# Performance work log

Hardware: AMD Instinct MI355X
Metric: run time of the kernel (lower is better)

The kernel has to match this reference:

```python
import jax, jax.numpy as jnp
import numpy as np

T, B, F, H = 1024, 64, 256, 512


def setup_inputs() -> dict:
    key = jax.random.key(0)
    k0, k1, k2 = jax.random.split(key, 3)
    s_i = 1.0 / np.sqrt(F)  # lecun_normal-ish scaling for input kernels
    s_h = 1.0 / np.sqrt(H)  # orthogonal-ish scaling for recurrent kernels
    return {
        "x": jax.random.normal(k0, (T, B, F), jnp.float32),
        "h0": jnp.zeros((B, H), jnp.float32),  # flax initialize_carry -> zeros
        "Wi": jax.random.normal(k1, (F, 3 * H), jnp.float32) * s_i,   # [ir|iz|in]
        "bi": jnp.zeros((3 * H,), jnp.float32),
        "Wh": jax.random.normal(k2, (H, 3 * H), jnp.float32) * s_h,   # [hr|hz|hn]
        "bhn": jnp.zeros((H,), jnp.float32),  # only the 'n' hidden dense has bias
    }


def reference(x, h0, Wi, bi, Wh, bhn):
    # Precompute all input-to-hidden projections in one big GEMM (math-equivalent
    # to doing them per step inside the scan, but far more efficient).
    xg = jnp.einsum('tbf,fg->tbg', x, Wi) + bi  # (T, B, 3H)

    def step(h, xg_t):
        hg = h @ Wh                              # (B, 3H)
        xr, xz, xn = jnp.split(xg_t, 3, axis=-1)
        hr, hz, hn = jnp.split(hg, 3, axis=-1)
        r = jax.nn.sigmoid(xr + hr)
        z = jax.nn.sigmoid(xz + hz)
        n = jnp.tanh(xn + r * (hn + bhn))
        h_new = (1.0 - z) * n + z * h            # flax GRUCell update
        return h_new, h_new

    _, ys = jax.lax.scan(step, h0, xg)
    return ys  # (T, B, H); final carry == ys[-1]
```

## Files before the change

kernel.cpp:

```cpp
#include <hip/hip_runtime.h>
#include <stdint.h>

#define NB 32

typedef __attribute__((ext_vector_type(8))) short short8;
typedef __attribute__((ext_vector_type(4))) float floatx4;

__device__ __forceinline__ unsigned short f2bf(float f) {
  unsigned u = __float_as_uint(f);
  u += 0x7fff + ((u >> 16) & 1);
  return (unsigned short)(u >> 16);
}
__device__ __forceinline__ float bf2f(unsigned short s) {
  return __uint_as_float(((unsigned)s) << 16);
}

__device__ __forceinline__ short8 load_frag_agent(const unsigned short* p) {
  union { unsigned long long u[2]; short8 s; } v;
  v.u[0] = __hip_atomic_load((const unsigned long long*)p,
                             __ATOMIC_RELAXED, __HIP_MEMORY_SCOPE_AGENT);
  v.u[1] = __hip_atomic_load((const unsigned long long*)(p + 4),
                             __ATOMIC_RELAXED, __HIP_MEMORY_SCOPE_AGENT);
  return v.s;
}

__global__ __launch_bounds__(256) void prep_kernel(
    const float* __restrict__ x, const float* __restrict__ h0,
    const float* __restrict__ Wi, const float* __restrict__ Wh,
    unsigned short* __restrict__ xbf, unsigned short* __restrict__ wit,
    unsigned short* __restrict__ wht, unsigned short* __restrict__ hbf,
    unsigned int* __restrict__ ctr) {
  int i = blockIdx.x * 256 + threadIdx.x;
  if (i < 4194304) {
    float4 v = ((const float4*)x)[i];
    ushort4 o;
    o.x = f2bf(v.x); o.y = f2bf(v.y); o.z = f2bf(v.z); o.w = f2bf(v.w);
    ((ushort4*)xbf)[i] = o;
  } else if (i < 4587520) {
    int j = i - 4194304;
    int n = j >> 8, k = j & 255;
    wit[j] = f2bf(Wi[(size_t)k * 1536 + n]);
  } else if (i < 5373952) {
    int j = i - 4587520;
    int n = j >> 9, k = j & 511;
    wht[j] = f2bf(Wh[(size_t)k * 1536 + n]);
  } else if (i < 5406720) {
    int j = i - 5373952;
    __hip_atomic_store(&hbf[j], f2bf(h0[j]),
                       __ATOMIC_RELAXED, __HIP_MEMORY_SCOPE_AGENT);
  } else if (i == 5406720) {
    __hip_atomic_store(ctr, 0u, __ATOMIC_RELAXED, __HIP_MEMORY_SCOPE_AGENT);
  }
}

__global__ __launch_bounds__(256, 2) void gemm_xg(
    const unsigned short* __restrict__ A,
    const unsigned short* __restrict__ BT,
    const float* __restrict__ bi,
    unsigned short* __restrict__ C) {
  __shared__ __align__(16) unsigned short lA[128 * 72];
  __shared__ __align__(16) unsigned short lB[128 * 72];
  const int tid = threadIdx.x;
  const int w = tid >> 6, lane = tid & 63;
  const int wm = w >> 1, wn = w & 1;
  const int q = lane >> 4, l16 = lane & 15;
  const int bx = blockIdx.x, by = blockIdx.y;

  floatx4 acc[4][4];
#pragma unroll
  for (int a = 0; a < 4; ++a)
#pragma unroll
    for (int b = 0; b < 4; ++b) acc[a][b] = (floatx4){0.f, 0.f, 0.f, 0.f};

  for (int kt = 0; kt < 4; ++kt) {
    if (kt) __syncthreads();
#pragma unroll
    for (int i = 0; i < 4; ++i) {
      int c = tid + i * 256;
      int r = c >> 3, kk = (c & 7) * 8;
      *(uint4*)&lA[r * 72 + kk] =
          *(const uint4*)&A[(size_t)(bx * 128 + r) * 256 + kt * 64 + kk];
      *(uint4*)&lB[r * 72 + kk] =
          *(const uint4*)&BT[(size_t)(by * 128 + r) * 256 + kt * 64 + kk];
    }
    __syncthreads();
#pragma unroll
    for (int ks = 0; ks < 2; ++ks) {
      const int kk = ks * 32 + q * 8;
      short8 af[4], bf[4];
#pragma unroll
      for (int rm = 0; rm < 4; ++rm)
        af[rm] = *(const short8*)&lA[(wm * 64 + rm * 16 + l16) * 72 + kk];
#pragma unroll
      for (int cn = 0; cn < 4; ++cn)
        bf[cn] = *(const short8*)&lB[(wn * 64 + cn * 16 + l16) * 72 + kk];
#pragma unroll
      for (int rm = 0; rm < 4; ++rm)
#pragma unroll
        for (int cn = 0; cn < 4; ++cn)
          acc[rm][cn] = __builtin_amdgcn_mfma_f32_16x16x32_bf16(
              af[rm], bf[cn], acc[rm][cn], 0, 0, 0);
    }
  }
#pragma unroll
  for (int cn = 0; cn < 4; ++cn) {
    const int col = by * 128 + wn * 64 + cn * 16 + l16;
    const float bic = bi[col];
#pragma unroll
    for (int rm = 0; rm < 4; ++rm)
#pragma unroll
      for (int r = 0; r < 4; ++r) {
        const int row = bx * 128 + wm * 64 + rm * 16 + q * 4 + r;
        C[(size_t)row * 1536 + col] = f2bf(acc[rm][cn][r] + bic);
      }
  }
}

__global__ __launch_bounds__(256, 1) void scan_kernel(
    const unsigned short* __restrict__ xg,
    const unsigned short* __restrict__ wht,
    const float* __restrict__ h0, const float* __restrict__ bhn,
    float* __restrict__ ys,
    unsigned short* __restrict__ hbf,
    unsigned int* __restrict__ ctr) {
  const int tid = threadIdx.x;
  const int w = tid >> 6, lane = tid & 63;
  const int q = lane >> 4, l16 = lane & 15;
  const int i0 = blockIdx.x * 16;

  short8 bfr[3][16];
#pragma unroll
  for (int g = 0; g < 3; ++g)
#pragma unroll
    for (int s = 0; s < 16; ++s)
      bfr[g][s] = *(const short8*)
          &wht[(size_t)(g * 512 + i0 + l16) * 512 + s * 32 + q * 8];

  const int dim = i0 + l16;
  const float bhn_c = bhn[dim];
  const int bc0 = w * 16 + q * 4;
  const int ba = w * 16 + l16;

  float hreg[4];
#pragma unroll
  for (int r = 0; r < 4; ++r) hreg[r] = h0[(size_t)(bc0 + r) * 512 + dim];

  float xgv[3][4];
#pragma unroll
  for (int r = 0; r < 4; ++r) {
    size_t xb = (size_t)(bc0 + r) * 1536 + dim;
    xgv[0][r] = bf2f(xg[xb]);
    xgv[1][r] = bf2f(xg[xb + 512]);
    xgv[2][r] = bf2f(xg[xb + 1024]);
  }

  for (int t = 0; t < 1024; ++t) {
    const unsigned short* hsrc = hbf + (size_t)(t & 1) * 32768;
    unsigned short* hdst = hbf + (size_t)((t + 1) & 1) * 32768;

    short8 af[16];
#pragma unroll
    for (int s = 0; s < 16; ++s)
      af[s] = load_frag_agent(&hsrc[(size_t)ba * 512 + s * 32 + q * 8]);

    floatx4 a0 = {0.f, 0.f, 0.f, 0.f};
    floatx4 a1 = {0.f, 0.f, 0.f, 0.f};
    floatx4 a2 = {0.f, 0.f, 0.f, 0.f};
#pragma unroll
    for (int s = 0; s < 16; ++s) {
      a0 = __builtin_amdgcn_mfma_f32_16x16x32_bf16(af[s], bfr[0][s], a0, 0, 0, 0);
      a1 = __builtin_amdgcn_mfma_f32_16x16x32_bf16(af[s], bfr[1][s], a1, 0, 0, 0);
      a2 = __builtin_amdgcn_mfma_f32_16x16x32_bf16(af[s], bfr[2][s], a2, 0, 0, 0);
    }

#pragma unroll
    for (int r = 0; r < 4; ++r) {
      const int bc = bc0 + r;
      float rg = 1.f / (1.f + __expf(-(xgv[0][r] + a0[r])));
      float zg = 1.f / (1.f + __expf(-(xgv[1][r] + a1[r])));
      float pre = xgv[2][r] + rg * (a2[r] + bhn_c);
      pre = fminf(fmaxf(pre, -15.f), 15.f);
      float e2 = __expf(2.f * pre);
      float ng = (e2 - 1.f) / (e2 + 1.f);
      float hnew = (1.f - zg) * ng + zg * hreg[r];
      hreg[r] = hnew;
      __hip_atomic_store(&hdst[(size_t)bc * 512 + dim], f2bf(hnew),
                         __ATOMIC_RELAXED, __HIP_MEMORY_SCOPE_AGENT);
      ys[((size_t)t * 64 + bc) * 512 + dim] = hnew;
    }

    if (t != 1023) {
#pragma unroll
      for (int r = 0; r < 4; ++r) {
        size_t xb = ((size_t)(t + 1) * 64 + bc0 + r) * 1536 + dim;
        xgv[0][r] = bf2f(xg[xb]);
        xgv[1][r] = bf2f(xg[xb + 512]);
        xgv[2][r] = bf2f(xg[xb + 1024]);
      }
      __syncthreads();
      if (tid == 0) {
        __hip_atomic_fetch_add(ctr, 1u, __ATOMIC_RELAXED,
                               __HIP_MEMORY_SCOPE_AGENT);
        const unsigned tgt = (unsigned)NB * (unsigned)(t + 1);
        while (__hip_atomic_load(ctr, __ATOMIC_RELAXED,
                                 __HIP_MEMORY_SCOPE_AGENT) < tgt) {}
      }
      __syncthreads();
    }
  }
}

extern "C" void kernel_launch(void* const* d_in, const int* in_sizes, int n_in,
                              void* d_out, int out_size, void* d_ws, size_t ws_size,
                              hipStream_t stream) {
  const float* x   = (const float*)d_in[0];
  const float* h0  = (const float*)d_in[1];
  const float* Wi  = (const float*)d_in[2];
  const float* bi  = (const float*)d_in[3];
  const float* Wh  = (const float*)d_in[4];
  const float* bhn = (const float*)d_in[5];
  float* ys = (float*)d_out;

  char* ws = (char*)d_ws;
  unsigned short* xg  = (unsigned short*)(ws);
  unsigned short* xbf = (unsigned short*)(ws + 201326592);
  unsigned short* wit = (unsigned short*)(ws + 234881024);
  unsigned short* wht = (unsigned short*)(ws + 235667456);
  unsigned short* hbf = (unsigned short*)(ws + 237240320);
  unsigned int*   ctr = (unsigned int*)(ws + 237371392);

  prep_kernel<<<21121, 256, 0, stream>>>(x, h0, Wi, Wh, xbf, wit, wht, hbf, ctr);
  gemm_xg<<<dim3(512, 12), 256, 0, stream>>>(xbf, wit, bi, xg);
  scan_kernel<<<NB, 256, 0, stream>>>(xg, wht, h0, bhn, ys, hbf, ctr);
}
```

Baseline: 6.119 ms.

## Use release-flag grid barrier and overlap xg prefetch and ys stores with MFMA

```diff
diff --git a/kernel.cpp b/kernel.cpp
--- a/kernel.cpp
+++ b/kernel.cpp
@@ -29,7 +29,7 @@
     const float* __restrict__ Wi, const float* __restrict__ Wh,
     unsigned short* __restrict__ xbf, unsigned short* __restrict__ wit,
     unsigned short* __restrict__ wht, unsigned short* __restrict__ hbf,
-    unsigned int* __restrict__ ctr) {
+    unsigned int* __restrict__ ctr, unsigned int* __restrict__ go) {
   int i = blockIdx.x * 256 + threadIdx.x;
   if (i < 4194304) {
     float4 v = ((const float4*)x)[i];
@@ -50,6 +50,7 @@
                        __ATOMIC_RELAXED, __HIP_MEMORY_SCOPE_AGENT);
   } else if (i == 5406720) {
     __hip_atomic_store(ctr, 0u, __ATOMIC_RELAXED, __HIP_MEMORY_SCOPE_AGENT);
+    __hip_atomic_store(go, 0u, __ATOMIC_RELAXED, __HIP_MEMORY_SCOPE_AGENT);
   }
 }
 
@@ -122,7 +123,7 @@
     const float* __restrict__ h0, const float* __restrict__ bhn,
     float* __restrict__ ys,
     unsigned short* __restrict__ hbf,
-    unsigned int* __restrict__ ctr) {
+    unsigned int* __restrict__ ctr, unsigned int* __restrict__ go) {
   const int tid = threadIdx.x;
   const int w = tid >> 6, lane = tid & 63;
   const int q = lane >> 4, l16 = lane & 15;
@@ -145,13 +146,13 @@
 #pragma unroll
   for (int r = 0; r < 4; ++r) hreg[r] = h0[(size_t)(bc0 + r) * 512 + dim];
 
-  float xgv[3][4];
+  float xcur[3][4];
 #pragma unroll
   for (int r = 0; r < 4; ++r) {
     size_t xb = (size_t)(bc0 + r) * 1536 + dim;
-    xgv[0][r] = bf2f(xg[xb]);
-    xgv[1][r] = bf2f(xg[xb + 512]);
-    xgv[2][r] = bf2f(xg[xb + 1024]);
+    xcur[0][r] = bf2f(xg[xb]);
+    xcur[1][r] = bf2f(xg[xb + 512]);
+    xcur[2][r] = bf2f(xg[xb + 1024]);
   }
 
   for (int t = 0; t < 1024; ++t) {
@@ -162,6 +163,22 @@
 #pragma unroll
     for (int s = 0; s < 16; ++s)
       af[s] = load_frag_agent(&hsrc[(size_t)ba * 512 + s * 32 + q * 8]);
+
+    float xnext[3][4];
+    if (t != 1023) {
+#pragma unroll
+      for (int r = 0; r < 4; ++r) {
+        size_t xb = ((size_t)(t + 1) * 64 + bc0 + r) * 1536 + dim;
+        xnext[0][r] = bf2f(xg[xb]);
+        xnext[1][r] = bf2f(xg[xb + 512]);
+        xnext[2][r] = bf2f(xg[xb + 1024]);
+      }
+    }
+    if (t != 0) {
+#pragma unroll
+      for (int r = 0; r < 4; ++r)
+        ys[((size_t)(t - 1) * 64 + bc0 + r) * 512 + dim] = hreg[r];
+    }
 
     floatx4 a0 = {0.f, 0.f, 0.f, 0.f};
     floatx4 a1 = {0.f, 0.f, 0.f, 0.f};
@@ -176,9 +193,9 @@
 #pragma unroll
     for (int r = 0; r < 4; ++r) {
       const int bc = bc0 + r;
-      float rg = 1.f / (1.f + __expf(-(xgv[0][r] + a0[r])));
-      float zg = 1.f / (1.f + __expf(-(xgv[1][r] + a1[r])));
-      float pre = xgv[2][r] + rg * (a2[r] + bhn_c);
+      float rg = 1.f / (1.f + __expf(-(xcur[0][r] + a0[r])));
+      float zg = 1.f / (1.f + __expf(-(xcur[1][r] + a1[r])));
+      float pre = xcur[2][r] + rg * (a2[r] + bhn_c);
       pre = fminf(fmaxf(pre, -15.f), 15.f);
       float e2 = __expf(2.f * pre);
       float ng = (e2 - 1.f) / (e2 + 1.f);
@@ -186,28 +203,33 @@
       hreg[r] = hnew;
       __hip_atomic_store(&hdst[(size_t)bc * 512 + dim], f2bf(hnew),
                          __ATOMIC_RELAXED, __HIP_MEMORY_SCOPE_AGENT);
-      ys[((size_t)t * 64 + bc) * 512 + dim] = hnew;
     }
 
     if (t != 1023) {
-#pragma unroll
-      for (int r = 0; r < 4; ++r) {
-        size_t xb = ((size_t)(t + 1) * 64 + bc0 + r) * 1536 + dim;
-        xgv[0][r] = bf2f(xg[xb]);
-        xgv[1][r] = bf2f(xg[xb + 512]);
-        xgv[2][r] = bf2f(xg[xb + 1024]);
+      __syncthreads();
+      if (tid == 0) {
+        const unsigned tgt = (unsigned)NB * (unsigned)(t + 1);
+        unsigned old = __hip_atomic_fetch_add(ctr, 1u, __ATOMIC_RELAXED,
+                                              __HIP_MEMORY_SCOPE_AGENT);
+        if (old == tgt - 1u) {
+          __hip_atomic_store(go, (unsigned)(t + 1), __ATOMIC_RELAXED,
+                             __HIP_MEMORY_SCOPE_AGENT);
+        } else {
+          while (__hip_atomic_load(go, __ATOMIC_RELAXED,
+                                   __HIP_MEMORY_SCOPE_AGENT) < (unsigned)(t + 1))
+            __builtin_amdgcn_s_sleep(1);
+        }
       }
       __syncthreads();
-      if (tid == 0) {
-        __hip_atomic_fetch_add(ctr, 1u, __ATOMIC_RELAXED,
-                               __HIP_MEMORY_SCOPE_AGENT);
-        const unsigned tgt = (unsigned)NB * (unsigned)(t + 1);
-        while (__hip_atomic_load(ctr, __ATOMIC_RELAXED,
-                                 __HIP_MEMORY_SCOPE_AGENT) < tgt) {}
-      }
-      __syncthreads();
-    }
-  }
+#pragma unroll
+      for (int g = 0; g < 3; ++g)
+#pragma unroll
+        for (int r = 0; r < 4; ++r) xcur[g][r] = xnext[g][r];
+    }
+  }
+#pragma unroll
+  for (int r = 0; r < 4; ++r)
+    ys[((size_t)1023 * 64 + bc0 + r) * 512 + dim] = hreg[r];
 }
 
 extern "C" void kernel_launch(void* const* d_in, const int* in_sizes, int n_in,
@@ -228,8 +250,9 @@
   unsigned short* wht = (unsigned short*)(ws + 235667456);
   unsigned short* hbf = (unsigned short*)(ws + 237240320);
   unsigned int*   ctr = (unsigned int*)(ws + 237371392);
-
-  prep_kernel<<<21121, 256, 0, stream>>>(x, h0, Wi, Wh, xbf, wit, wht, hbf, ctr);
+  unsigned int*   go  = (unsigned int*)(ws + 237371520);
+
+  prep_kernel<<<21121, 256, 0, stream>>>(x, h0, Wi, Wh, xbf, wit, wht, hbf, ctr, go);
   gemm_xg<<<dim3(512, 12), 256, 0, stream>>>(xbf, wit, bi, xg);
-  scan_kernel<<<NB, 256, 0, stream>>>(xg, wht, h0, bhn, ys, hbf, ctr);
-}
+  scan_kernel<<<NB, 256, 0, stream>>>(xg, wht, h0, bhn, ys, hbf, ctr, go);
+}
```

Result: slower. 6.517 ms (+6.5%).
